# Optimization experiments

Measured on AMD Instinct MI355X. Metric: run time of the kernel, lower is better.

Reference implementation:

```python
import jax, jax.numpy as jnp
import numpy as np

S, N, D, H = 4096, 16384, 768, 768  # n_slots, n_inputs, feature_size(=dim), mlp hidden
ITERS = 3
SCALE = D ** -0.5
LN_EPS = 1e-5  # torch LayerNorm default


def _ln(x, g, b):
    m = jnp.mean(x, axis=-1, keepdims=True)
    v = jnp.var(x, axis=-1, keepdims=True)
    return (x - m) * jax.lax.rsqrt(v + LN_EPS) * g + b


def setup_inputs() -> dict:
    key = jax.random.key(0)
    ks = jax.random.split(key, 16)
    w = lambda k, shp: jax.random.normal(k, shp, dtype=jnp.float32) * 0.02
    return {
        "cand_feat": jax.random.normal(ks[0], (S, D), dtype=jnp.float32),
        "pano_feat": jax.random.normal(ks[1], (N, D), dtype=jnp.float32),
        "Wq": w(ks[2], (D, D)), "bq": jnp.zeros((D,), jnp.float32),
        "Wk": w(ks[3], (D, D)), "bk": jnp.zeros((D,), jnp.float32),
        "Wv": w(ks[4], (D, D)), "bv": jnp.zeros((D,), jnp.float32),
        "W_ih": w(ks[5], (3 * D, D)), "b_ih": jnp.zeros((3 * D,), jnp.float32),
        "W_hh": w(ks[6], (3 * D, D)), "b_hh": jnp.zeros((3 * D,), jnp.float32),
        "W1": w(ks[7], (H, D)), "b1": jnp.zeros((H,), jnp.float32),
        "W2": w(ks[8], (D, H)), "b2": jnp.zeros((D,), jnp.float32),
        "g_in": jnp.ones((D,), jnp.float32), "be_in": jnp.zeros((D,), jnp.float32),
        "g_sl": jnp.ones((D,), jnp.float32), "be_sl": jnp.zeros((D,), jnp.float32),
        "g_ff": jnp.ones((D,), jnp.float32), "be_ff": jnp.zeros((D,), jnp.float32),
    }


def reference(cand_feat, pano_feat, Wq, bq, Wk, bk, Wv, bv,
              W_ih, b_ih, W_hh, b_hh, W1, b1, W2, b2,
              g_in, be_in, g_sl, be_sl, g_ff, be_ff):
    # dropout layers act as identity at inference
    slots = cand_feat                       # [S, D]
    pano = _ln(pano_feat, g_in, be_in)      # [N, D]
    k = pano @ Wk.T + bk                    # [N, D]
    v = pano @ Wv.T + bv                    # [N, D]
    for _ in range(ITERS):
        slots_prev = slots
        q = _ln(slots, g_sl, be_sl) @ Wq.T + bq          # [S, D]
        dots = jnp.einsum('id,jd->ij', q, k) * SCALE     # [S, N]
        attn = jax.nn.softmax(dots, axis=1)
        updates = jnp.einsum('jd,ij->id', v, attn)       # [S, D]
        # torch.nn.GRUCell(updates, slots_prev)
        gx = updates @ W_ih.T + b_ih                     # [S, 3D]
        gh = slots_prev @ W_hh.T + b_hh                  # [S, 3D]
        xr, xz, xn = jnp.split(gx, 3, axis=-1)
        hr, hz, hn = jnp.split(gh, 3, axis=-1)
        r = jax.nn.sigmoid(xr + hr)
        z = jax.nn.sigmoid(xz + hz)
        n = jnp.tanh(xn + r * hn)
        h = (1.0 - z) * n + z * slots_prev               # [S, D]
        ff = _ln(h, g_ff, be_ff)
        slots = h + (jax.nn.relu(ff @ W1.T + b1) @ W2.T + b2)
    return slots
```

## Files before the change

kernel.cpp:

```cpp
#include <hip/hip_runtime.h>
#include <cstdint>
#include <cstddef>

typedef __bf16 bf16;
typedef __bf16 bf16x8 __attribute__((ext_vector_type(8)));
typedef __bf16 bf16x4 __attribute__((ext_vector_type(4)));
typedef float f32x4 __attribute__((ext_vector_type(4)));

#define S_DIM 4096
#define N_DIM 16384
#define D_DIM 768
#define NCHUNK 4096
#define KSLICE 1024

static constexpr float SCALE = 0.03608439182435161f;

__device__ inline void gl_lds16(const void* g, void* l) {
  __builtin_amdgcn_global_load_lds((const __attribute__((address_space(1))) void*)g,
                                   (__attribute__((address_space(3))) void*)l, 16, 0, 0);
}

struct GemmArgs {
  const bf16* A; const bf16* B;
  const float* bias;
  float* outF; bf16* outB;
  const float* res;
  float* lsum;
  int M, N, K, lda, ldb;
  float scale;
};

template<int EPIL>
__device__ __forceinline__ void gemm_core(const GemmArgs& g, const int bm, const int bn,
                                          bf16* sA, bf16* sB) {
  const int tid  = threadIdx.x;
  const int wave = tid >> 6;
  const int lane = tid & 63;
  const int quad = lane >> 4;
  const int l15  = lane & 15;
  const int wm = (wave >> 1) * 64;
  const int wn = (wave & 1) * 64;

  f32x4 acc[4][4];
#pragma unroll
  for (int t = 0; t < 4; ++t)
#pragma unroll
    for (int u = 0; u < 4; ++u) acc[t][u] = (f32x4){0.f, 0.f, 0.f, 0.f};

  const int s0 = wave * 64 + lane;
  const int s1 = 256 + s0;
  const size_t lda = (size_t)g.lda, ldb = (size_t)g.ldb;
  const bf16* gA0 = g.A + (size_t)(bm + (s0 >> 2)) * lda + (s0 & 3) * 8;
  const bf16* gA1 = g.A + (size_t)(bm + (s1 >> 2)) * lda + (s1 & 3) * 8;
  const bf16* gB0 = g.B + (size_t)(bn + (s0 >> 2)) * ldb + (s0 & 3) * 8;
  const bf16* gB1 = g.B + (size_t)(bn + (s1 >> 2)) * ldb + (s1 & 3) * 8;
  bf16* lA0 = sA + s0 * 8;  bf16* lA1 = sA + s1 * 8;
  bf16* lB0 = sB + s0 * 8;  bf16* lB1 = sB + s1 * 8;

  for (int k0 = 0; k0 < g.K; k0 += 32) {
    __syncthreads();
    gl_lds16(gA0 + k0, lA0);
    gl_lds16(gA1 + k0, lA1);
    gl_lds16(gB0 + k0, lB0);
    gl_lds16(gB1 + k0, lB1);
    __syncthreads();
    bf16x8 af[4], bv[4];
#pragma unroll
    for (int t = 0; t < 4; ++t)
      af[t] = *(const bf16x8*)(sA + (wm + t * 16 + l15) * 32 + quad * 8);
#pragma unroll
    for (int u = 0; u < 4; ++u)
      bv[u] = *(const bf16x8*)(sB + (wn + u * 16 + l15) * 32 + quad * 8);
#pragma unroll
    for (int t = 0; t < 4; ++t)
#pragma unroll
      for (int u = 0; u < 4; ++u)
        acc[t][u] = __builtin_amdgcn_mfma_f32_16x16x32_bf16(af[t], bv[u], acc[t][u], 0, 0, 0);
  }

  const int ldc = g.N;
#pragma unroll
  for (int t = 0; t < 4; ++t) {
    const int rbase = bm + wm + t * 16 + quad * 4;
    if (EPIL == 2) {
      float rsum[4] = {0.f, 0.f, 0.f, 0.f};
#pragma unroll
      for (int u = 0; u < 4; ++u) {
        const int col = bn + wn + u * 16 + l15;
#pragma unroll
        for (int r = 0; r < 4; ++r) {
          float e = __expf(acc[t][u][r] * g.scale);
          g.outB[(size_t)(rbase + r) * ldc + col] = (bf16)e;
          rsum[r] += e;
        }
      }
#pragma unroll
      for (int m = 1; m < 16; m <<= 1)
#pragma unroll
        for (int r = 0; r < 4; ++r) rsum[r] += __shfl_xor(rsum[r], m, 64);
      if (l15 == 0)
#pragma unroll
        for (int r = 0; r < 4; ++r) atomicAdd(&g.lsum[rbase + r], rsum[r]);
    } else {
#pragma unroll
      for (int u = 0; u < 4; ++u) {
        const int col = bn + wn + u * 16 + l15;
        const float cbias = (EPIL == 0 || EPIL == 4 || EPIL == 5) ? g.bias[col] : 0.f;
#pragma unroll
        for (int r = 0; r < 4; ++r) {
          const size_t idx = (size_t)(rbase + r) * ldc + col;
          const float v = acc[t][u][r];
          if (EPIL == 0) g.outB[idx] = (bf16)(v + cbias);
          else if (EPIL == 4) { float x = v + cbias; g.outB[idx] = (bf16)(x > 0.f ? x : 0.f); }
          else if (EPIL == 5) g.outF[idx] = v + cbias + g.res[idx];
          else if (EPIL == 6) g.outF[idx] += v;
          else if (EPIL == 7) g.outB[idx] = (bf16)(v + g.bias[rbase + r]);
          else if (EPIL == 8) g.outF[idx] = v;
        }
      }
    }
  }
}

#define GEMM_SHARED __shared__ __align__(16) bf16 sA[128 * 32]; __shared__ __align__(16) bf16 sB[128 * 32]

__global__ __launch_bounds__(256) void k_dots(GemmArgs g) {
  GEMM_SHARED; gemm_core<2>(g, blockIdx.y * 128, blockIdx.x * 128, sA, sB);
}
__global__ __launch_bounds__(256) void k_qgemm(GemmArgs g) {
  GEMM_SHARED; gemm_core<0>(g, blockIdx.y * 128, blockIdx.x * 128, sA, sB);
}
__global__ __launch_bounds__(256) void k_kgemm(GemmArgs g) {
  GEMM_SHARED; gemm_core<0>(g, blockIdx.y * 128, blockIdx.x * 128, sA, sB);
}
__global__ __launch_bounds__(256) void k_vtgemm(GemmArgs g) {
  GEMM_SHARED; gemm_core<7>(g, blockIdx.y * 128, blockIdx.x * 128, sA, sB);
}
__global__ __launch_bounds__(256) void k_relu(GemmArgs g) {
  GEMM_SHARED; gemm_core<4>(g, blockIdx.y * 128, blockIdx.x * 128, sA, sB);
}
__global__ __launch_bounds__(256) void k_resid(GemmArgs g) {
  GEMM_SHARED; gemm_core<5>(g, blockIdx.y * 128, blockIdx.x * 128, sA, sB);
}
__global__ __launch_bounds__(256) void k_dual(GemmArgs a, GemmArgs b, int split) {
  GEMM_SHARED;
  if ((int)blockIdx.x < split) gemm_core<0>(a, blockIdx.y * 128, blockIdx.x * 128, sA, sB);
  else                         gemm_core<0>(b, blockIdx.y * 128, (blockIdx.x - split) * 128, sA, sB);
}

struct UpdArgs {
  const bf16* A; const bf16* B;
  float* out[4];
  int lda, ldb;
};
template<int INIT>
__global__ __launch_bounds__(256) void k_updsplit(UpdArgs u) {
  GEMM_SHARED;
  const int z = blockIdx.z;
  GemmArgs g{};
  g.A = u.A + (size_t)z * KSLICE;
  g.B = u.B + (size_t)z * KSLICE;
  g.outF = u.out[z];
  g.M = S_DIM; g.N = D_DIM; g.K = KSLICE; g.lda = u.lda; g.ldb = u.ldb;
  gemm_core<INIT ? 8 : 6>(g, blockIdx.y * 128, blockIdx.x * 128, sA, sB);
}

__global__ void reduce4_div_k(const float* __restrict__ b0, const float* __restrict__ b1,
                              const float* __restrict__ b2, const float* __restrict__ b3,
                              const float* __restrict__ lsum, bf16* __restrict__ out) {
  const int idx = blockIdx.x * 256 + threadIdx.x;
  const int row = idx / 192;
  const float inv = 1.0f / lsum[row];
  float4 v0 = ((const float4*)b0)[idx];
  float4 v1 = ((const float4*)b1)[idx];
  float4 v2 = ((const float4*)b2)[idx];
  float4 v3 = ((const float4*)b3)[idx];
  bf16x4 y;
  y[0] = (bf16)((v0.x + v1.x + v2.x + v3.x) * inv);
  y[1] = (bf16)((v0.y + v1.y + v2.y + v3.y) * inv);
  y[2] = (bf16)((v0.z + v1.z + v2.z + v3.z) * inv);
  y[3] = (bf16)((v0.w + v1.w + v2.w + v3.w) * inv);
  ((bf16x4*)out)[idx] = y;
}

__global__ void ln_stats_k(const float* __restrict__ X, float2* __restrict__ st) {
  const int row  = blockIdx.x * 4 + (threadIdx.x >> 6);
  const int lane = threadIdx.x & 63;
  const float4* xr = (const float4*)(X + (size_t)row * 768);
  float s = 0.f, ss = 0.f;
#pragma unroll
  for (int i = 0; i < 3; ++i) {
    float4 v = xr[lane + 64 * i];
    s  += v.x + v.y + v.z + v.w;
    ss += v.x * v.x + v.y * v.y + v.z * v.z + v.w * v.w;
  }
#pragma unroll
  for (int m = 1; m < 64; m <<= 1) { s += __shfl_xor(s, m, 64); ss += __shfl_xor(ss, m, 64); }
  if (lane == 0) {
    float mean = s * (1.f / 768.f);
    float var  = ss * (1.f / 768.f) - mean * mean;
    st[row] = make_float2(mean, rsqrtf(var + 1e-5f));
  }
}

__global__ void ln_apply_k(const float* __restrict__ X, const float2* __restrict__ st,
                           const float* __restrict__ gam, const float* __restrict__ bet,
                           bf16* __restrict__ Y) {
  const int idx = blockIdx.x * 256 + threadIdx.x;
  const int row = idx / 192, c4 = idx % 192;
  const float2 s = st[row];
  float4 x  = ((const float4*)(X + (size_t)row * 768))[c4];
  float4 g4 = ((const float4*)gam)[c4];
  float4 b4 = ((const float4*)bet)[c4];
  bf16x4 y;
  y[0] = (bf16)((x.x - s.x) * s.y * g4.x + b4.x);
  y[1] = (bf16)((x.y - s.x) * s.y * g4.y + b4.y);
  y[2] = (bf16)((x.z - s.x) * s.y * g4.z + b4.z);
  y[3] = (bf16)((x.w - s.x) * s.y * g4.w + b4.w);
  ((bf16x4*)(Y + (size_t)row * 768))[c4] = y;
}

__global__ void cvt_k(const float* __restrict__ X, bf16* __restrict__ Y) {
  const int i = blockIdx.x * 256 + threadIdx.x;
  float4 v = ((const float4*)X)[i];
  bf16x4 y;
  y[0] = (bf16)v.x; y[1] = (bf16)v.y; y[2] = (bf16)v.z; y[3] = (bf16)v.w;
  ((bf16x4*)Y)[i] = y;
}

__device__ inline float gru1(float xr, float xz, float xn, float hr, float hz, float hn, float sp) {
  float r = 1.f / (1.f + __expf(-(xr + hr)));
  float z = 1.f / (1.f + __expf(-(xz + hz)));
  float n = tanhf(xn + r * hn);
  return (1.f - z) * n + z * sp;
}

__global__ void gru_gate_k(const bf16* __restrict__ gx, const bf16* __restrict__ gh,
                           const float* __restrict__ slots, float* __restrict__ h) {
  const int idx = blockIdx.x * 256 + threadIdx.x;
  const int row = idx / 192, c4 = idx % 192;
  const bf16x4* gxr = (const bf16x4*)(gx + (size_t)row * 2304);
  const bf16x4* ghr = (const bf16x4*)(gh + (size_t)row * 2304);
  bf16x4 xr = gxr[c4], xz = gxr[192 + c4], xn = gxr[384 + c4];
  bf16x4 hr = ghr[c4], hz = ghr[192 + c4], hn = ghr[384 + c4];
  float4 sp = ((const float4*)(slots + (size_t)row * 768))[c4];
  float4 o;
  o.x = gru1((float)xr[0], (float)xz[0], (float)xn[0], (float)hr[0], (float)hz[0], (float)hn[0], sp.x);
  o.y = gru1((float)xr[1], (float)xz[1], (float)xn[1], (float)hr[1], (float)hz[1], (float)hn[1], sp.y);
  o.z = gru1((float)xr[2], (float)xz[2], (float)xn[2], (float)hr[2], (float)hz[2], (float)hn[2], sp.z);
  o.w = gru1((float)xr[3], (float)xz[3], (float)xn[3], (float)hr[3], (float)hz[3], (float)hn[3], sp.w);
  ((float4*)(h + (size_t)row * 768))[c4] = o;
}

extern "C" void kernel_launch(void* const* d_in, const int* in_sizes, int n_in,
                              void* d_out, int out_size, void* d_ws, size_t ws_size,
                              hipStream_t stream) {
  (void)in_sizes; (void)n_in; (void)out_size; (void)ws_size;
  const float* cand  = (const float*)d_in[0];
  const float* pano  = (const float*)d_in[1];
  const float* Wq  = (const float*)d_in[2];  const float* bq  = (const float*)d_in[3];
  const float* Wk  = (const float*)d_in[4];  const float* bk  = (const float*)d_in[5];
  const float* Wv  = (const float*)d_in[6];  const float* bv  = (const float*)d_in[7];
  const float* Wih = (const float*)d_in[8];  const float* bih = (const float*)d_in[9];
  const float* Whh = (const float*)d_in[10]; const float* bhh = (const float*)d_in[11];
  const float* W1  = (const float*)d_in[12]; const float* b1  = (const float*)d_in[13];
  const float* W2  = (const float*)d_in[14]; const float* b2  = (const float*)d_in[15];
  const float* g_in = (const float*)d_in[16]; const float* be_in = (const float*)d_in[17];
  const float* g_sl = (const float*)d_in[18]; const float* be_sl = (const float*)d_in[19];
  const float* g_ff = (const float*)d_in[20]; const float* be_ff = (const float*)d_in[21];

  const size_t WU = (size_t)D_DIM * D_DIM;

  char* base = (char*)d_ws;
  size_t off = 0;
  auto alloc = [&](size_t bytes) -> void* {
    void* r = base + off;
    off = (off + bytes + 255) & ~(size_t)255;
    return r;
  };

  bf16* wq_bf  = (bf16*)alloc(WU * 2);
  bf16* wk_bf  = (bf16*)alloc(WU * 2);
  bf16* wv_bf  = (bf16*)alloc(WU * 2);
  bf16* wih_bf = (bf16*)alloc(3 * WU * 2);
  bf16* whh_bf = (bf16*)alloc(3 * WU * 2);
  bf16* w1_bf  = (bf16*)alloc(WU * 2);
  bf16* w2_bf  = (bf16*)alloc(WU * 2);
  bf16* k_bf   = (bf16*)alloc((size_t)N_DIM * D_DIM * 2);
  bf16* vt_bf  = (bf16*)alloc((size_t)N_DIM * D_DIM * 2);
  float* slots = (float*)alloc((size_t)S_DIM * D_DIM * 4);
  bf16* slots_bf = (bf16*)alloc((size_t)S_DIM * D_DIM * 2);
  float2* statsP = (float2*)alloc((size_t)N_DIM * 8);
  float2* statsS = (float2*)alloc((size_t)S_DIM * 8);
  bf16* slotsln = (bf16*)alloc((size_t)S_DIM * D_DIM * 2);
  bf16* q_bf    = (bf16*)alloc((size_t)S_DIM * D_DIM * 2);
  bf16* upd_bf  = (bf16*)alloc((size_t)S_DIM * D_DIM * 2);
  bf16* hln_bf  = (bf16*)alloc((size_t)S_DIM * D_DIM * 2);
  bf16* m1_bf   = (bf16*)alloc((size_t)S_DIM * D_DIM * 2);
  float* lsum   = (float*)alloc((size_t)S_DIM * 4);
  float* hbuf   = (float*)alloc((size_t)S_DIM * D_DIM * 4);
  const size_t PCH = (size_t)S_DIM * NCHUNK * 2;
  const size_t UBF = (size_t)S_DIM * D_DIM * 4;
  const size_t GSZ = (size_t)S_DIM * 3 * D_DIM * 2;
  char* arena = (char*)alloc(PCH + 3 * UBF);
  bf16* panoln = (bf16*)arena;
  bf16* Pchunk = (bf16*)arena;
  float* buf0 = hbuf;
  float* buf1 = (float*)(arena + PCH);
  float* buf2 = (float*)(arena + PCH + UBF);
  float* buf3 = (float*)(arena + PCH + 2 * UBF);
  bf16* gx = (bf16*)(arena + PCH);
  bf16* gh = (bf16*)(arena + PCH + GSZ);

  cvt_k<<<dim3(WU / 1024), 256, 0, stream>>>(Wq, wq_bf);
  cvt_k<<<dim3(WU / 1024), 256, 0, stream>>>(Wk, wk_bf);
  cvt_k<<<dim3(WU / 1024), 256, 0, stream>>>(Wv, wv_bf);
  cvt_k<<<dim3(3 * WU / 1024), 256, 0, stream>>>(Wih, wih_bf);
  cvt_k<<<dim3(3 * WU / 1024), 256, 0, stream>>>(Whh, whh_bf);
  cvt_k<<<dim3(WU / 1024), 256, 0, stream>>>(W1, w1_bf);
  cvt_k<<<dim3(WU / 1024), 256, 0, stream>>>(W2, w2_bf);

  ln_stats_k<<<dim3(N_DIM / 4), 256, 0, stream>>>(pano, statsP);
  ln_apply_k<<<dim3(N_DIM * 192 / 256), 256, 0, stream>>>(pano, statsP, g_in, be_in, panoln);

  {
    GemmArgs ak{};
    ak.A = panoln; ak.B = wk_bf; ak.bias = bk; ak.outB = k_bf;
    ak.M = N_DIM; ak.N = D_DIM; ak.K = D_DIM; ak.lda = D_DIM; ak.ldb = D_DIM;
    k_kgemm<<<dim3(6, 128), 256, 0, stream>>>(ak);
    GemmArgs av{};
    av.A = wv_bf; av.B = panoln; av.bias = bv; av.outB = vt_bf;
    av.M = D_DIM; av.N = N_DIM; av.K = D_DIM; av.lda = D_DIM; av.ldb = D_DIM;
    k_vtgemm<<<dim3(128, 6), 256, 0, stream>>>(av);
  }

  hipMemcpyAsync(slots, cand, (size_t)S_DIM * D_DIM * 4, hipMemcpyDeviceToDevice, stream);
  cvt_k<<<dim3(S_DIM * D_DIM / 1024), 256, 0, stream>>>(cand, slots_bf);

  for (int iter = 0; iter < 3; ++iter) {
    ln_stats_k<<<dim3(S_DIM / 4), 256, 0, stream>>>(slots, statsS);
    ln_apply_k<<<dim3(S_DIM * 192 / 256), 256, 0, stream>>>(slots, statsS, g_sl, be_sl, slotsln);
    GemmArgs aq{};
    aq.A = slotsln; aq.B = wq_bf; aq.bias = bq; aq.outB = q_bf;
    aq.M = S_DIM; aq.N = D_DIM; aq.K = D_DIM; aq.lda = D_DIM; aq.ldb = D_DIM;
    k_qgemm<<<dim3(6, 32), 256, 0, stream>>>(aq);

    hipMemsetAsync(lsum, 0, (size_t)S_DIM * 4, stream);
    for (int c = 0; c < N_DIM / NCHUNK; ++c) {
      GemmArgs ad{};
      ad.A = q_bf; ad.B = k_bf + (size_t)c * NCHUNK * D_DIM;
      ad.outB = Pchunk; ad.lsum = lsum; ad.scale = SCALE;
      ad.M = S_DIM; ad.N = NCHUNK; ad.K = D_DIM; ad.lda = D_DIM; ad.ldb = D_DIM;
      k_dots<<<dim3(NCHUNK / 128, S_DIM / 128), 256, 0, stream>>>(ad);

      UpdArgs au{};
      au.A = Pchunk; au.B = vt_bf + (size_t)c * NCHUNK;
      au.out[0] = buf0; au.out[1] = buf1; au.out[2] = buf2; au.out[3] = buf3;
      au.lda = NCHUNK; au.ldb = N_DIM;
      if (c == 0) k_updsplit<1><<<dim3(6, 32, 4), 256, 0, stream>>>(au);
      else        k_updsplit<0><<<dim3(6, 32, 4), 256, 0, stream>>>(au);
    }
    reduce4_div_k<<<dim3(S_DIM * 192 / 256), 256, 0, stream>>>(buf0, buf1, buf2, buf3, lsum, upd_bf);

    {
      GemmArgs agx{};
      agx.A = upd_bf; agx.B = wih_bf; agx.bias = bih; agx.outB = gx;
      agx.M = S_DIM; agx.N = 3 * D_DIM; agx.K = D_DIM; agx.lda = D_DIM; agx.ldb = D_DIM;
      GemmArgs agh{};
      agh.A = slots_bf; agh.B = whh_bf; agh.bias = bhh; agh.outB = gh;
      agh.M = S_DIM; agh.N = 3 * D_DIM; agh.K = D_DIM; agh.lda = D_DIM; agh.ldb = D_DIM;
      k_dual<<<dim3(36, 32), 256, 0, stream>>>(agx, agh, 18);
    }
    gru_gate_k<<<dim3(S_DIM * 192 / 256), 256, 0, stream>>>(gx, gh, slots, hbuf);

    ln_stats_k<<<dim3(S_DIM / 4), 256, 0, stream>>>(hbuf, statsS);
    ln_apply_k<<<dim3(S_DIM * 192 / 256), 256, 0, stream>>>(hbuf, statsS, g_ff, be_ff, hln_bf);
    GemmArgs am1{};
    am1.A = hln_bf; am1.B = w1_bf; am1.bias = b1; am1.outB = m1_bf;
    am1.M = S_DIM; am1.N = D_DIM; am1.K = D_DIM; am1.lda = D_DIM; am1.ldb = D_DIM;
    k_relu<<<dim3(6, 32), 256, 0, stream>>>(am1);
    GemmArgs am2{};
    am2.A = m1_bf; am2.B = w2_bf; am2.bias = b2; am2.res = hbuf;
    am2.outF = (iter == 2) ? (float*)d_out : slots;
    am2.M = S_DIM; am2.N = D_DIM; am2.K = D_DIM; am2.lda = D_DIM; am2.ldb = D_DIM;
    k_resid<<<dim3(6, 32), 256, 0, stream>>>(am2);

    if (iter < 2)
      cvt_k<<<dim3(S_DIM * D_DIM / 1024), 256, 0, stream>>>(slots, slots_bf);
  }
}
```

Measured before the change: 2.062 ms.

## Use FP8 for attention probabilities and V in the update GEMM

Softmax numerators and the transposed V projection are stored as FP8 instead of bf16, and the attention-times-V GEMM now uses the fp8 MFMA instruction. The chunk size grows to 8192 with 8 K-splits, and the split partials are kept in bf16 instead of fp32. The aim is to halve the traffic for the probability matrix and V and to use the faster fp8 matrix path, at the cost of accuracy. FP8 unnormalised exponentials and bf16 partial sums (read-modify-write across chunks) risk exceeding the tolerance.

```diff
diff --git a/kernel.cpp b/kernel.cpp
--- a/kernel.cpp
+++ b/kernel.cpp
@@ -6,12 +6,14 @@
 typedef __bf16 bf16x8 __attribute__((ext_vector_type(8)));
 typedef __bf16 bf16x4 __attribute__((ext_vector_type(4)));
 typedef float f32x4 __attribute__((ext_vector_type(4)));
+typedef long long i64;
 
 #define S_DIM 4096
 #define N_DIM 16384
 #define D_DIM 768
-#define NCHUNK 4096
-#define KSLICE 1024
+#define NCHUNK 8192
+#define NZ 8
+#define KSLICE (NCHUNK / NZ)
 
 static constexpr float SCALE = 0.03608439182435161f;
 
@@ -20,10 +22,15 @@
                                    (__attribute__((address_space(3))) void*)l, 16, 0, 0);
 }
 
+__device__ inline unsigned char to_fp8(float x) {
+  int p = __builtin_amdgcn_cvt_pk_fp8_f32(x, x, 0, false);
+  return (unsigned char)(p & 0xff);
+}
+
 struct GemmArgs {
   const bf16* A; const bf16* B;
   const float* bias;
-  float* outF; bf16* outB;
+  float* outF; bf16* outB; unsigned char* outP8;
   const float* res;
   float* lsum;
   int M, N, K, lda, ldb;
@@ -82,7 +89,7 @@
 #pragma unroll
   for (int t = 0; t < 4; ++t) {
     const int rbase = bm + wm + t * 16 + quad * 4;
-    if (EPIL == 2) {
+    if (EPIL == 10) {
       float rsum[4] = {0.f, 0.f, 0.f, 0.f};
 #pragma unroll
       for (int u = 0; u < 4; ++u) {
@@ -90,7 +97,7 @@
 #pragma unroll
         for (int r = 0; r < 4; ++r) {
           float e = __expf(acc[t][u][r] * g.scale);
-          g.outB[(size_t)(rbase + r) * ldc + col] = (bf16)e;
+          g.outP8[(size_t)(rbase + r) * ldc + col] = to_fp8(e);
           rsum[r] += e;
         }
       }
@@ -113,9 +120,7 @@
           if (EPIL == 0) g.outB[idx] = (bf16)(v + cbias);
           else if (EPIL == 4) { float x = v + cbias; g.outB[idx] = (bf16)(x > 0.f ? x : 0.f); }
           else if (EPIL == 5) g.outF[idx] = v + cbias + g.res[idx];
-          else if (EPIL == 6) g.outF[idx] += v;
-          else if (EPIL == 7) g.outB[idx] = (bf16)(v + g.bias[rbase + r]);
-          else if (EPIL == 8) g.outF[idx] = v;
+          else if (EPIL == 9) g.outP8[idx] = to_fp8(v + g.bias[rbase + r]);
         }
       }
     }
@@ -125,7 +130,7 @@
 #define GEMM_SHARED __shared__ __align__(16) bf16 sA[128 * 32]; __shared__ __align__(16) bf16 sB[128 * 32]
 
 __global__ __launch_bounds__(256) void k_dots(GemmArgs g) {
-  GEMM_SHARED; gemm_core<2>(g, blockIdx.y * 128, blockIdx.x * 128, sA, sB);
+  GEMM_SHARED; gemm_core<10>(g, blockIdx.y * 128, blockIdx.x * 128, sA, sB);
 }
 __global__ __launch_bounds__(256) void k_qgemm(GemmArgs g) {
   GEMM_SHARED; gemm_core<0>(g, blockIdx.y * 128, blockIdx.x * 128, sA, sB);
@@ -134,7 +139,7 @@
   GEMM_SHARED; gemm_core<0>(g, blockIdx.y * 128, blockIdx.x * 128, sA, sB);
 }
 __global__ __launch_bounds__(256) void k_vtgemm(GemmArgs g) {
-  GEMM_SHARED; gemm_core<7>(g, blockIdx.y * 128, blockIdx.x * 128, sA, sB);
+  GEMM_SHARED; gemm_core<9>(g, blockIdx.y * 128, blockIdx.x * 128, sA, sB);
 }
 __global__ __launch_bounds__(256) void k_relu(GemmArgs g) {
   GEMM_SHARED; gemm_core<4>(g, blockIdx.y * 128, blockIdx.x * 128, sA, sB);
@@ -148,38 +153,93 @@
   else                         gemm_core<0>(b, blockIdx.y * 128, (blockIdx.x - split) * 128, sA, sB);
 }
 
-struct UpdArgs {
-  const bf16* A; const bf16* B;
-  float* out[4];
+struct F8Args {
+  const unsigned char* A; const unsigned char* B;
+  bf16* out;
   int lda, ldb;
 };
+
 template<int INIT>
-__global__ __launch_bounds__(256) void k_updsplit(UpdArgs u) {
-  GEMM_SHARED;
+__global__ __launch_bounds__(256) void k_updsplit(F8Args u) {
+  __shared__ __align__(16) unsigned char sA[128 * 32];
+  __shared__ __align__(16) unsigned char sB[128 * 32];
   const int z = blockIdx.z;
-  GemmArgs g{};
-  g.A = u.A + (size_t)z * KSLICE;
-  g.B = u.B + (size_t)z * KSLICE;
-  g.outF = u.out[z];
-  g.M = S_DIM; g.N = D_DIM; g.K = KSLICE; g.lda = u.lda; g.ldb = u.ldb;
-  gemm_core<INIT ? 8 : 6>(g, blockIdx.y * 128, blockIdx.x * 128, sA, sB);
-}
-
-__global__ void reduce4_div_k(const float* __restrict__ b0, const float* __restrict__ b1,
-                              const float* __restrict__ b2, const float* __restrict__ b3,
-                              const float* __restrict__ lsum, bf16* __restrict__ out) {
+  const unsigned char* A = u.A + (size_t)z * KSLICE;
+  const unsigned char* B = u.B + (size_t)z * KSLICE;
+  bf16* out = u.out + (size_t)z * S_DIM * D_DIM;
+
+  const int tid  = threadIdx.x;
+  const int wave = tid >> 6;
+  const int lane = tid & 63;
+  const int quad = lane >> 4;
+  const int l15  = lane & 15;
+  const int bm = blockIdx.y * 128;
+  const int bn = blockIdx.x * 128;
+  const int wm = (wave >> 1) * 64;
+  const int wn = (wave & 1) * 64;
+
+  f32x4 acc[4][4];
+#pragma unroll
+  for (int t = 0; t < 4; ++t)
+#pragma unroll
+    for (int u2 = 0; u2 < 4; ++u2) acc[t][u2] = (f32x4){0.f, 0.f, 0.f, 0.f};
+
+  const int s0 = wave * 64 + lane;
+  const size_t lda = (size_t)u.lda, ldb = (size_t)u.ldb;
+  const unsigned char* gA0 = A + (size_t)(bm + (s0 >> 1)) * lda + (s0 & 1) * 16;
+  const unsigned char* gB0 = B + (size_t)(bn + (s0 >> 1)) * ldb + (s0 & 1) * 16;
+  unsigned char* lA0 = sA + s0 * 16;
+  unsigned char* lB0 = sB + s0 * 16;
+
+  for (int k0 = 0; k0 < KSLICE; k0 += 32) {
+    __syncthreads();
+    gl_lds16(gA0 + k0, lA0);
+    gl_lds16(gB0 + k0, lB0);
+    __syncthreads();
+    i64 af[4], bv[4];
+#pragma unroll
+    for (int t = 0; t < 4; ++t)
+      af[t] = *(const i64*)(sA + (wm + t * 16 + l15) * 32 + quad * 8);
+#pragma unroll
+    for (int u2 = 0; u2 < 4; ++u2)
+      bv[u2] = *(const i64*)(sB + (wn + u2 * 16 + l15) * 32 + quad * 8);
+#pragma unroll
+    for (int t = 0; t < 4; ++t)
+#pragma unroll
+      for (int u2 = 0; u2 < 4; ++u2)
+        acc[t][u2] = __builtin_amdgcn_mfma_f32_16x16x32_fp8_fp8(af[t], bv[u2], acc[t][u2], 0, 0, 0);
+  }
+
+#pragma unroll
+  for (int t = 0; t < 4; ++t) {
+    const int rbase = bm + wm + t * 16 + quad * 4;
+#pragma unroll
+    for (int u2 = 0; u2 < 4; ++u2) {
+      const int col = bn + wn + u2 * 16 + l15;
+#pragma unroll
+      for (int r = 0; r < 4; ++r) {
+        const size_t idx = (size_t)(rbase + r) * D_DIM + col;
+        if (INIT) out[idx] = (bf16)acc[t][u2][r];
+        else      out[idx] = (bf16)((float)out[idx] + acc[t][u2][r]);
+      }
+    }
+  }
+}
+
+__global__ void reduce8_div_k(const bf16* __restrict__ bufs, const float* __restrict__ lsum,
+                              bf16* __restrict__ out) {
   const int idx = blockIdx.x * 256 + threadIdx.x;
   const int row = idx / 192;
   const float inv = 1.0f / lsum[row];
-  float4 v0 = ((const float4*)b0)[idx];
-  float4 v1 = ((const float4*)b1)[idx];
-  float4 v2 = ((const float4*)b2)[idx];
-  float4 v3 = ((const float4*)b3)[idx];
+  float s0 = 0.f, s1 = 0.f, s2 = 0.f, s3 = 0.f;
+#pragma unroll
+  for (int z = 0; z < NZ; ++z) {
+    bf16x4 v = ((const bf16x4*)(bufs + (size_t)z * S_DIM * D_DIM))[idx];
+    s0 += (float)v[0]; s1 += (float)v[1]; s2 += (float)v[2]; s3 += (float)v[3];
+  }
   bf16x4 y;
-  y[0] = (bf16)((v0.x + v1.x + v2.x + v3.x) * inv);
-  y[1] = (bf16)((v0.y + v1.y + v2.y + v3.y) * inv);
-  y[2] = (bf16)((v0.z + v1.z + v2.z + v3.z) * inv);
-  y[3] = (bf16)((v0.w + v1.w + v2.w + v3.w) * inv);
+  y[0] = (bf16)(s0 * inv); y[1] = (bf16)(s1 * inv);
+  y[2] = (bf16)(s2 * inv); y[3] = (bf16)(s3 * inv);
   ((bf16x4*)out)[idx] = y;
 }
 
@@ -287,7 +347,7 @@
   bf16* w1_bf  = (bf16*)alloc(WU * 2);
   bf16* w2_bf  = (bf16*)alloc(WU * 2);
   bf16* k_bf   = (bf16*)alloc((size_t)N_DIM * D_DIM * 2);
-  bf16* vt_bf  = (bf16*)alloc((size_t)N_DIM * D_DIM * 2);
+  unsigned char* vt_f8 = (unsigned char*)alloc((size_t)N_DIM * D_DIM);
   float* slots = (float*)alloc((size_t)S_DIM * D_DIM * 4);
   bf16* slots_bf = (bf16*)alloc((size_t)S_DIM * D_DIM * 2);
   float2* statsP = (float2*)alloc((size_t)N_DIM * 8);
@@ -299,18 +359,14 @@
   bf16* m1_bf   = (bf16*)alloc((size_t)S_DIM * D_DIM * 2);
   float* lsum   = (float*)alloc((size_t)S_DIM * 4);
   float* hbuf   = (float*)alloc((size_t)S_DIM * D_DIM * 4);
-  const size_t PCH = (size_t)S_DIM * NCHUNK * 2;
-  const size_t UBF = (size_t)S_DIM * D_DIM * 4;
-  const size_t GSZ = (size_t)S_DIM * 3 * D_DIM * 2;
-  char* arena = (char*)alloc(PCH + 3 * UBF);
+  const size_t PCH = (size_t)S_DIM * NCHUNK;
+  const size_t PBF = (size_t)NZ * S_DIM * D_DIM * 2;
+  char* arena = (char*)alloc(PCH + PBF);
   bf16* panoln = (bf16*)arena;
-  bf16* Pchunk = (bf16*)arena;
-  float* buf0 = hbuf;
-  float* buf1 = (float*)(arena + PCH);
-  float* buf2 = (float*)(arena + PCH + UBF);
-  float* buf3 = (float*)(arena + PCH + 2 * UBF);
-  bf16* gx = (bf16*)(arena + PCH);
-  bf16* gh = (bf16*)(arena + PCH + GSZ);
+  unsigned char* Pchunk = (unsigned char*)arena;
+  bf16* pbufs = (bf16*)(arena + PCH);
+  bf16* gx = (bf16*)arena;
+  bf16* gh = (bf16*)(arena + PCH);
 
   cvt_k<<<dim3(WU / 1024), 256, 0, stream>>>(Wq, wq_bf);
   cvt_k<<<dim3(WU / 1024), 256, 0, stream>>>(Wk, wk_bf);
@@ -322,14 +378,13 @@
 
   ln_stats_k<<<dim3(N_DIM / 4), 256, 0, stream>>>(pano, statsP);
   ln_apply_k<<<dim3(N_DIM * 192 / 256), 256, 0, stream>>>(pano, statsP, g_in, be_in, panoln);
-
   {
     GemmArgs ak{};
     ak.A = panoln; ak.B = wk_bf; ak.bias = bk; ak.outB = k_bf;
     ak.M = N_DIM; ak.N = D_DIM; ak.K = D_DIM; ak.lda = D_DIM; ak.ldb = D_DIM;
     k_kgemm<<<dim3(6, 128), 256, 0, stream>>>(ak);
     GemmArgs av{};
-    av.A = wv_bf; av.B = panoln; av.bias = bv; av.outB = vt_bf;
+    av.A = wv_bf; av.B = panoln; av.bias = bv; av.outP8 = vt_f8;
     av.M = D_DIM; av.N = N_DIM; av.K = D_DIM; av.lda = D_DIM; av.ldb = D_DIM;
     k_vtgemm<<<dim3(128, 6), 256, 0, stream>>>(av);
   }
@@ -349,18 +404,17 @@
     for (int c = 0; c < N_DIM / NCHUNK; ++c) {
       GemmArgs ad{};
       ad.A = q_bf; ad.B = k_bf + (size_t)c * NCHUNK * D_DIM;
-      ad.outB = Pchunk; ad.lsum = lsum; ad.scale = SCALE;
+      ad.outP8 = Pchunk; ad.lsum = lsum; ad.scale = SCALE;
       ad.M = S_DIM; ad.N = NCHUNK; ad.K = D_DIM; ad.lda = D_DIM; ad.ldb = D_DIM;
       k_dots<<<dim3(NCHUNK / 128, S_DIM / 128), 256, 0, stream>>>(ad);
 
-      UpdArgs au{};
-      au.A = Pchunk; au.B = vt_bf + (size_t)c * NCHUNK;
-      au.out[0] = buf0; au.out[1] = buf1; au.out[2] = buf2; au.out[3] = buf3;
-      au.lda = NCHUNK; au.ldb = N_DIM;
-      if (c == 0) k_updsplit<1><<<dim3(6, 32, 4), 256, 0, stream>>>(au);
-      else        k_updsplit<0><<<dim3(6, 32, 4), 256, 0, stream>>>(au);
+      F8Args au{};
+      au.A = Pchunk; au.B = vt_f8 + (size_t)c * NCHUNK;
+      au.out = pbufs; au.lda = NCHUNK; au.ldb = N_DIM;
+      if (c == 0) k_updsplit<1><<<dim3(6, 32, NZ), 256, 0, stream>>>(au);
+      else        k_updsplit<0><<<dim3(6, 32, NZ), 256, 0, stream>>>(au);
     }
-    reduce4_div_k<<<dim3(S_DIM * 192 / 256), 256, 0, stream>>>(buf0, buf1, buf2, buf3, lsum, upd_bf);
+    reduce8_div_k<<<dim3(S_DIM * 192 / 256), 256, 0, stream>>>(pbufs, lsum, upd_bf);
 
     {
       GemmArgs agx{};
```

After: 1.903 ms. 7.7% less time.
